# Kernel tuning notes

Measured on AMD Instinct MI355X. Metric: run time of the kernel, lower is better.

The kernel has to match this reference:

```python
import jax, jax.numpy as jnp
import numpy as np

USER_NUM = 100_000
ITEM_NUM = 50_000
N = USER_NUM + ITEM_NUM          # total nodes in the bipartite graph
HIDDEN = 64
LAYERS = 3
BATCH = 4096
NNZ = 4_800_000                  # ~avg degree 32


def setup_inputs() -> dict:
    key = jax.random.key(0)
    ks = jax.random.split(key, 7)
    emb = jax.random.normal(ks[0], (N, HIDDEN), dtype=jnp.float32) * 0.02
    rows = jax.random.randint(ks[1], (NNZ,), 0, N, dtype=jnp.int32)
    cols = jax.random.randint(ks[2], (NNZ,), 0, N, dtype=jnp.int32)
    # normalized-laplacian-like positive values, scaled ~ 1/avg_degree
    vals = jax.random.uniform(ks[3], (NNZ,), dtype=jnp.float32) * (1.0 / 32.0)
    user = jax.random.randint(ks[4], (BATCH,), 0, USER_NUM, dtype=jnp.int32)
    pos = jax.random.randint(ks[5], (BATCH,), USER_NUM, N, dtype=jnp.int32)
    neg = jax.random.randint(ks[6], (BATCH,), USER_NUM, N, dtype=jnp.int32)
    return {"emb": emb, "vals": vals, "rows": rows, "cols": cols,
            "user": user, "pos": pos, "neg": neg}


def _spmm(rows, cols, vals, x):
    # sparse [N,N] @ dense [N,d] in COO form: gather + scale + segment-sum
    return jax.ops.segment_sum(vals[:, None] * x[cols], rows, num_segments=N)


def reference(emb, vals, rows, cols, user, pos, neg):
    # layer-0 gathers
    user_acc = emb[user]
    pos_acc = emb[pos]
    neg_acc = emb[neg]
    e = emb
    for _ in range(LAYERS):
        e = _spmm(rows, cols, vals, e)
        user_acc = user_acc + e[user]
        pos_acc = pos_acc + e[pos]
        neg_acc = neg_acc + e[neg]
    denom = jnp.float32(LAYERS + 1)
    u = user_acc / denom   # mean over stacked layers
    p = pos_acc / denom
    n = neg_acc / denom
    pos_logits = jnp.einsum('id,id->i', u, p)
    neg_logits = jnp.einsum('id,id->i', u, n)
    # -log(sigmoid(x)) == -log_sigmoid(x) (numerically stable)
    loss = -jax.nn.log_sigmoid(pos_logits - neg_logits)
    return loss.sum()
```

## Files before the change

kernel.cpp:

```cpp
#include <hip/hip_runtime.h>

#define HIDDEN 64
#define PAD 96
#define CHUNK 8192
#define NBMAX 640
#define CAP 9600
#define S_SCALE 64.0f
#define INV_S 0.015625f

typedef unsigned int uint;
typedef unsigned char uchar;

__device__ __forceinline__ ushort f2bf(float f) {
    uint u = __float_as_uint(f);
    u = (u + 0x7FFFu + ((u >> 16) & 1u)) >> 16;
    return (ushort)u;
}
__device__ __forceinline__ float bf2f(ushort h) {
    return __uint_as_float(((uint)h) << 16);
}

#if __has_builtin(__builtin_amdgcn_cvt_pk_fp8_f32) && __has_builtin(__builtin_amdgcn_cvt_pk_f32_fp8)
#define FP8_HW 1
#else
#define FP8_HW 0
#endif

__device__ __forceinline__ uint enc8(float a, float b, float c, float d) {
#if FP8_HW
    int r = __builtin_amdgcn_cvt_pk_fp8_f32(a, b, 0, false);
    r = __builtin_amdgcn_cvt_pk_fp8_f32(c, d, r, true);
    return (uint)r;
#else
    auto enc1 = [](float x) -> uint {
        uint u = __float_as_uint(x);
        uint s = (u >> 24) & 0x80u;
        float af = fabsf(x);
        if (af < 0.015625f) return s;
        if (af >= 448.f) return s | 0x7Eu;
        uint bits = u & 0x7FFFFFFFu;
        bits -= (120u << 23);
        uint r = (bits + 0x7FFFFu + ((bits >> 20) & 1u)) >> 20;
        if (r > 0x7Eu) r = 0x7Eu;
        return s | r;
    };
    return enc1(a) | (enc1(b) << 8) | (enc1(c) << 16) | (enc1(d) << 24);
#endif
}

__device__ __forceinline__ float4 dec8(uint u) {
#if FP8_HW
    auto lo = __builtin_amdgcn_cvt_pk_f32_fp8((int)u, false);
    auto hi = __builtin_amdgcn_cvt_pk_f32_fp8((int)u, true);
    return make_float4(lo[0], lo[1], hi[0], hi[1]);
#else
    auto dec1 = [](uint b) -> float {
        uint m = b & 0x7Fu;
        uint s = (b & 0x80u) << 24;
        uint bits = m ? (s | ((m + 960u) << 20)) : s;
        return __uint_as_float(bits);
    };
    return make_float4(dec1(u & 0xFF), dec1((u >> 8) & 0xFF),
                       dec1((u >> 16) & 0xFF), dec1((u >> 24) & 0xFF));
#endif
}


__global__ void __launch_bounds__(256) k_f2fp8(const float4* __restrict__ src,
                                               uint2* __restrict__ dst, int n8) {
    int i = blockIdx.x * blockDim.x + threadIdx.x;
    if (i >= n8) return;
    float4 f0 = src[2 * i], f1 = src[2 * i + 1];
    uint2 o;
    o.x = enc8(f0.x * S_SCALE, f0.y * S_SCALE, f0.z * S_SCALE, f0.w * S_SCALE);
    o.y = enc8(f1.x * S_SCALE, f1.y * S_SCALE, f1.z * S_SCALE, f1.w * S_SCALE);
    dst[i] = o;
}


__global__ void __launch_bounds__(512) k_stage(const int* __restrict__ rows,
                                               const int* __restrict__ cols,
                                               const float* __restrict__ vals,
                                               int* __restrict__ cursor,
                                               int2* __restrict__ staged,
                                               int nnz, int nb) {
    __shared__ int  hS[NBMAX];
    __shared__ int  lsS[NBMAX];
    __shared__ int  gsS[NBMAX];
    __shared__ int  lcS[NBMAX];
    __shared__ int  ps[512];
    __shared__ int2 stg[CHUNK];

    int t  = threadIdx.x;
    int cb = blockIdx.x * CHUNK;

    for (int k = t; k < nb; k += 512) hS[k] = 0;
    __syncthreads();

    int4 ra[4];
    #pragma unroll
    for (int j = 0; j < 4; ++j) {
        int idx = cb + j * 2048 + t * 4;
        int4 r4;
        if (idx + 3 < nnz) {
            r4 = *(const int4*)(rows + idx);
        } else {
            r4.x = (idx     < nnz) ? rows[idx]     : -1;
            r4.y = (idx + 1 < nnz) ? rows[idx + 1] : -1;
            r4.z = (idx + 2 < nnz) ? rows[idx + 2] : -1;
            r4.w = (idx + 3 < nnz) ? rows[idx + 3] : -1;
        }
        ra[j] = r4;
        if (r4.x >= 0) atomicAdd(&hS[r4.x >> 8], 1);
        if (r4.y >= 0) atomicAdd(&hS[r4.y >> 8], 1);
        if (r4.z >= 0) atomicAdd(&hS[r4.z >> 8], 1);
        if (r4.w >= 0) atomicAdd(&hS[r4.w >> 8], 1);
    }
    __syncthreads();

    int k0 = 2 * t, k1 = 2 * t + 1;
    int c0 = (k0 < nb) ? hS[k0] : 0;
    int c1 = (k1 < nb) ? hS[k1] : 0;
    ps[t] = c0 + c1;
    __syncthreads();
    for (int d = 1; d < 512; d <<= 1) {
        int p = (t >= d) ? ps[t - d] : 0;
        __syncthreads();
        ps[t] += p;
        __syncthreads();
    }
    int excl = ps[t] - (c0 + c1);
    if (k0 < nb) { lsS[k0] = excl;      gsS[k0] = atomicAdd(&cursor[k0], c0); }
    if (k1 < nb) { lsS[k1] = excl + c0; gsS[k1] = atomicAdd(&cursor[k1], c1); }
    __syncthreads();
    for (int k = t; k < nb; k += 512) lcS[k] = lsS[k];
    __syncthreads();

    #pragma unroll
    for (int j = 0; j < 4; ++j) {
        int idx = cb + j * 2048 + t * 4;
        int4 r4 = ra[j];
        int4 c4; float4 v4;
        if (idx + 3 < nnz) {
            c4 = *(const int4*)(cols + idx);
            v4 = *(const float4*)(vals + idx);
        } else {
            c4.x = (idx     < nnz) ? cols[idx]     : 0;
            c4.y = (idx + 1 < nnz) ? cols[idx + 1] : 0;
            c4.z = (idx + 2 < nnz) ? cols[idx + 2] : 0;
            c4.w = (idx + 3 < nnz) ? cols[idx + 3] : 0;
            v4.x = (idx     < nnz) ? vals[idx]     : 0.f;
            v4.y = (idx + 1 < nnz) ? vals[idx + 1] : 0.f;
            v4.z = (idx + 2 < nnz) ? vals[idx + 2] : 0.f;
            v4.w = (idx + 3 < nnz) ? vals[idx + 3] : 0.f;
        }
        if (r4.x >= 0) { int s = atomicAdd(&lcS[r4.x >> 8], 1);
            stg[s] = make_int2(c4.x | ((r4.x & 255) << 18), __float_as_int(v4.x)); }
        if (r4.y >= 0) { int s = atomicAdd(&lcS[r4.y >> 8], 1);
            stg[s] = make_int2(c4.y | ((r4.y & 255) << 18), __float_as_int(v4.y)); }
        if (r4.z >= 0) { int s = atomicAdd(&lcS[r4.z >> 8], 1);
            stg[s] = make_int2(c4.z | ((r4.z & 255) << 18), __float_as_int(v4.z)); }
        if (r4.w >= 0) { int s = atomicAdd(&lcS[r4.w >> 8], 1);
            stg[s] = make_int2(c4.w | ((r4.w & 255) << 18), __float_as_int(v4.w)); }
    }
    __syncthreads();

    int m_total = nnz - cb; if (m_total > CHUNK) m_total = CHUNK;
    for (int i = t; i < m_total; i += 512) {
        int2 e = stg[i];
        int lo = 0, hi = nb - 1;
        while (lo < hi) {
            int mid = (lo + hi + 1) >> 1;
            if (lsS[mid] <= i) lo = mid; else hi = mid - 1;
        }
        int k = lo;
        int pos = gsS[k] + (i - lsS[k]);
        if (pos < CAP) staged[(size_t)k * CAP + pos] = e;
    }
}

__global__ void __launch_bounds__(1024) k_fine(const int2* __restrict__ staged,
                                               const int* __restrict__ stagecnt,
                                               int* __restrict__ cols_ell,
                                               ushort* __restrict__ vals_ell,
                                               int* __restrict__ cnt, int n) {
    __shared__ int2 out[CAP];
    __shared__ int hist[256], rstart[256], cursor[256], s2[256];
    int k = blockIdx.x;
    int t = threadIdx.x;
    size_t s0 = (size_t)k * CAP;
    int ck = stagecnt[k]; if (ck > CAP) ck = CAP;
    if (t < 256) hist[t] = 0;
    __syncthreads();
    for (int i = t; i < ck; i += 1024)
        atomicAdd(&hist[((uint)staged[s0 + i].x) >> 18], 1);
    __syncthreads();
    if (t < 256) s2[t] = hist[t];
    __syncthreads();
    for (int d = 1; d < 256; d <<= 1) {
        int p = (t < 256 && t >= d) ? s2[t - d] : 0;
        __syncthreads();
        if (t < 256) s2[t] += p;
        __syncthreads();
    }
    if (t < 256) {
        int rs = s2[t] - hist[t];
        rstart[t] = rs;
        cursor[t] = rs;
        int row = (k << 8) + t;
        if (row < n) cnt[row] = hist[t];
    }
    __syncthreads();
    for (int i = t; i < ck; i += 1024) {
        int2 e = staged[s0 + i];
        int lr = ((uint)e.x) >> 18;
        int slot = atomicAdd(&cursor[lr], 1);
        if (slot < CAP) out[slot] = make_int2(e.x & 0x3FFFF, e.y);
    }
    __syncthreads();
    for (int idx = t; idx < 256 * PAD; idx += 1024) {
        int lr = idx / PAD, j = idx - lr * PAD;
        if (j < hist[lr]) {
            int row = (k << 8) + lr;
            int2 o = out[rstart[lr] + j];
            cols_ell[(size_t)row * PAD + j] = o.x;
            vals_ell[(size_t)row * PAD + j] = f2bf(__int_as_float(o.y));
        }
    }
}


__device__ __forceinline__ float4 spmm_row4(const int* __restrict__ cnt,
                                            const int* __restrict__ cols_ell,
                                            const ushort* __restrict__ vals_ell,
                                            const uchar* __restrict__ x,
                                            int row, int lane) {
    int len = cnt[row]; if (len > PAD) len = PAD;
    const int*    cbp = cols_ell + (size_t)row * PAD;
    const ushort* vbp = vals_ell + (size_t)row * PAD;
    int g4 = (lane & 15) * 4;
    int e = lane >> 4;
    float a0 = 0.f, a1 = 0.f, a2 = 0.f, a3 = 0.f;
    float b0 = 0.f, b1 = 0.f, b2 = 0.f, b3 = 0.f;
    for (int j0 = 0; j0 < len; j0 += 64) {
        int m = len - j0; if (m > 64) m = 64;
        int c = 0; float v = 0.f;
        if (lane < m) {
            c = cbp[j0 + lane];
            v = bf2f(vbp[j0 + lane]);
        }
        int steps = (m + 3) >> 2;
        int s = 0;
        for (; s + 1 < steps; s += 2) {
            int   i0 = 4 * s + e,  i1 = 4 * s + 4 + e;
            int   c0 = __shfl(c, i0); float v0 = __shfl(v, i0);
            int   c1 = __shfl(c, i1); float v1 = __shfl(v, i1);
            uint u0 = *(const uint*)(x + ((size_t)c0 << 6) + g4);
            uint u1 = *(const uint*)(x + ((size_t)c1 << 6) + g4);
            float4 x0 = dec8(u0);
            float4 x1 = dec8(u1);
            a0 += v0 * x0.x; a1 += v0 * x0.y; a2 += v0 * x0.z; a3 += v0 * x0.w;
            b0 += v1 * x1.x; b1 += v1 * x1.y; b2 += v1 * x1.z; b3 += v1 * x1.w;
        }
        if (s < steps) {
            int i0 = 4 * s + e;
            int c0 = __shfl(c, i0); float v0 = __shfl(v, i0);
            uint u0 = *(const uint*)(x + ((size_t)c0 << 6) + g4);
            float4 x0 = dec8(u0);
            a0 += v0 * x0.x; a1 += v0 * x0.y; a2 += v0 * x0.z; a3 += v0 * x0.w;
        }
    }
    a0 += b0; a1 += b1; a2 += b2; a3 += b3;
    a0 += __shfl_xor(a0, 16); a1 += __shfl_xor(a1, 16);
    a2 += __shfl_xor(a2, 16); a3 += __shfl_xor(a3, 16);
    a0 += __shfl_xor(a0, 32); a1 += __shfl_xor(a1, 32);
    a2 += __shfl_xor(a2, 32); a3 += __shfl_xor(a3, 32);
    return make_float4(a0, a1, a2, a3);
}

__global__ void __launch_bounds__(256) k_spmm(const int* __restrict__ cnt,
                                              const int* __restrict__ cols_ell,
                                              const ushort* __restrict__ vals_ell,
                                              const uchar* __restrict__ x,
                                              uchar* __restrict__ y, int n) {
    int row  = (int)((blockIdx.x * blockDim.x + threadIdx.x) >> 6);
    int lane = threadIdx.x & 63;
    if (row >= n) return;
    float4 a = spmm_row4(cnt, cols_ell, vals_ell, x, row, lane);
    if (lane < 16) {
        uint r = enc8(a.x, a.y, a.z, a.w);
        *(uint*)(y + ((size_t)row << 6) + lane * 4) = r;
    }
}

__global__ void __launch_bounds__(256) k_spmm_batch(const int* __restrict__ cnt,
                                                    const int* __restrict__ cols_ell,
                                                    const ushort* __restrict__ vals_ell,
                                                    const uchar* __restrict__ x,
                                                    const int* __restrict__ user,
                                                    const int* __restrict__ pos,
                                                    const int* __restrict__ neg,
                                                    int batch, float* __restrict__ acc) {
    int slot = (int)((blockIdx.x * blockDim.x + threadIdx.x) >> 6);
    int lane = threadIdx.x & 63;
    if (slot >= 3 * batch) return;
    int which = slot / batch, i = slot - which * batch;
    const int* sel = (which == 0) ? user : (which == 1 ? pos : neg);
    float4 a = spmm_row4(cnt, cols_ell, vals_ell, x, sel[i], lane);
    if (lane < 16) {
        float4* p = (float4*)(acc + (size_t)slot * HIDDEN + lane * 4);
        float4 old = *p;
        old.x += a.x * INV_S; old.y += a.y * INV_S;
        old.z += a.z * INV_S; old.w += a.w * INV_S;
        *p = old;
    }
}


__global__ void __launch_bounds__(256) k_gather0(const float* __restrict__ e,
                                                 const int* __restrict__ user,
                                                 const int* __restrict__ pos,
                                                 const int* __restrict__ neg,
                                                 int batch, float* __restrict__ acc) {
    int row  = (int)((blockIdx.x * blockDim.x + threadIdx.x) >> 6);
    int lane = threadIdx.x & 63;
    if (row >= 3 * batch) return;
    int which = row / batch, i = row - which * batch;
    const int* sel = (which == 0) ? user : (which == 1 ? pos : neg);
    int s = sel[i];
    acc[(size_t)row * HIDDEN + lane] = e[(size_t)s * HIDDEN + lane];
}

__global__ void __launch_bounds__(256) k_gather8(const uchar* __restrict__ e,
                                                 const int* __restrict__ user,
                                                 const int* __restrict__ pos,
                                                 const int* __restrict__ neg,
                                                 int batch, float* __restrict__ acc) {
    int t    = blockIdx.x * blockDim.x + threadIdx.x;
    int wv   = t >> 6;
    int lane = threadIdx.x & 63;
    int row  = wv * 4 + (lane >> 4);
    if (row >= 3 * batch) return;
    int which = row / batch, i = row - which * batch;
    const int* sel = (which == 0) ? user : (which == 1 ? pos : neg);
    int s = sel[i];
    int g4 = (lane & 15) * 4;
    uint u = *(const uint*)(e + ((size_t)s << 6) + g4);
    float4 d = dec8(u);
    float4* p = (float4*)(acc + (size_t)row * HIDDEN + g4);
    float4 old = *p;
    old.x += d.x * INV_S; old.y += d.y * INV_S;
    old.z += d.z * INV_S; old.w += d.w * INV_S;
    *p = old;
}


__global__ void __launch_bounds__(256) k_loss(const float* __restrict__ acc, int batch,
                                              float* __restrict__ out) {
    int i    = (int)((blockIdx.x * blockDim.x + threadIdx.x) >> 6);
    int lane = threadIdx.x & 63;
    if (i >= batch) return;
    float u  = acc[(size_t)i * HIDDEN + lane] * 0.25f;
    float p  = acc[(size_t)(i + batch) * HIDDEN + lane] * 0.25f;
    float nn = acc[(size_t)(i + 2 * batch) * HIDDEN + lane] * 0.25f;
    float sp = u * p, sn = u * nn;
    for (int d = 32; d > 0; d >>= 1) {
        sp += __shfl_down(sp, d);
        sn += __shfl_down(sn, d);
    }
    if (lane == 0) {
        float z = sn - sp;
        float loss = fmaxf(z, 0.f) + log1pf(expf(-fabsf(z)));
        atomicAdd(out, loss);
    }
}


extern "C" void kernel_launch(void* const* d_in, const int* in_sizes, int n_in,
                              void* d_out, int out_size, void* d_ws, size_t ws_size,
                              hipStream_t stream) {
    (void)n_in; (void)out_size; (void)ws_size;
    const float* emb  = (const float*)d_in[0];
    const float* vals = (const float*)d_in[1];
    const int*   rows = (const int*)d_in[2];
    const int*   cols = (const int*)d_in[3];
    const int*   user = (const int*)d_in[4];
    const int*   pos  = (const int*)d_in[5];
    const int*   neg  = (const int*)d_in[6];

    const int n     = in_sizes[0] / HIDDEN;
    const int nnz   = in_sizes[1];
    const int batch = in_sizes[4];

    const int nb   = (n + 255) >> 8;
    const int nblk = (nnz + CHUNK - 1) / CHUNK;

    auto align256 = [](size_t x) { return (x + 255) & ~(size_t)255; };
    char* w = (char*)d_ws;
    int*    cnt      = (int*)w;    w += align256(sizeof(int)    * (size_t)n);
    int*    cursor   = (int*)w;    w += align256(sizeof(int)    * (size_t)NBMAX);
    int*    cols_ell = (int*)w;    w += align256(sizeof(int)    * (size_t)n * PAD);
    ushort* vals_ell = (ushort*)w; w += align256(sizeof(ushort) * (size_t)n * PAD);
    uchar*  emb8     = (uchar*)w;  w += align256((size_t)n * HIDDEN);
    uchar*  e0       = (uchar*)w;  w += align256((size_t)n * HIDDEN);
    uchar*  e1       = (uchar*)w;  w += align256((size_t)n * HIDDEN);
    float*  acc      = (float*)w;  w += align256(sizeof(float)  * (size_t)3 * batch * HIDDEN);
    int2*   staged   = (int2*)w;   w += align256(sizeof(int2)   * (size_t)nb * CAP);

    float* out = (float*)d_out;

    const int B = 256;
    dim3 blk(B);
    int g_conv = (n * HIDDEN / 8 + B - 1) / B;
    int g_spmm = (n + 3) / 4;
    int g_gath = (3 * batch + 3) / 4;
    int g_g8   = ((3 * batch + 3) / 4 * 64 + B - 1) / B;
    int g_loss = (batch + 3) / 4;

    hipMemsetAsync(cursor, 0, sizeof(int) * (size_t)NBMAX, stream);
    k_stage<<<nblk, 512, 0, stream>>>(rows, cols, vals, cursor, staged, nnz, nb);
    k_fine<<<nb, 1024, 0, stream>>>(staged, cursor, cols_ell, vals_ell, cnt, n);

    k_f2fp8<<<g_conv, blk, 0, stream>>>((const float4*)emb, (uint2*)emb8, n * HIDDEN / 8);

    hipMemsetAsync(out, 0, sizeof(float), stream);

    k_gather0<<<g_gath, blk, 0, stream>>>(emb, user, pos, neg, batch, acc);
    k_spmm<<<g_spmm, blk, 0, stream>>>(cnt, cols_ell, vals_ell, emb8, e0, n);
    k_gather8<<<g_g8, blk, 0, stream>>>(e0, user, pos, neg, batch, acc);
    k_spmm<<<g_spmm, blk, 0, stream>>>(cnt, cols_ell, vals_ell, e0, e1, n);
    k_gather8<<<g_g8, blk, 0, stream>>>(e1, user, pos, neg, batch, acc);
    k_spmm_batch<<<g_gath, blk, 0, stream>>>(cnt, cols_ell, vals_ell, e1, user, pos, neg, batch, acc);

    k_loss<<<g_loss, blk, 0, stream>>>(acc, batch, out);
}
```

Before: 325.0 us.

## Shrink staged COO entries to uint meta plus bf16 value, widen stage blocks

The staging kernel now converts values to bf16 early and writes them in a separate ushort array next to a uint metadata array, instead of int2 pairs. This cuts the bytes written and read through the intermediate staged buffer and the shared memory it uses. The stage kernel runs with 1024 threads and two int4 loads per thread instead of 512 threads and four. The SpMM inner loop is unrolled to four gathers per iteration to expose more memory-level parallelism, at the cost of more registers.

```diff
diff --git a/kernel.cpp b/kernel.cpp
--- a/kernel.cpp
+++ b/kernel.cpp
@@ -78,29 +78,31 @@
 }
 
 
-__global__ void __launch_bounds__(512) k_stage(const int* __restrict__ rows,
-                                               const int* __restrict__ cols,
-                                               const float* __restrict__ vals,
-                                               int* __restrict__ cursor,
-                                               int2* __restrict__ staged,
-                                               int nnz, int nb) {
-    __shared__ int  hS[NBMAX];
-    __shared__ int  lsS[NBMAX];
-    __shared__ int  gsS[NBMAX];
-    __shared__ int  lcS[NBMAX];
-    __shared__ int  ps[512];
-    __shared__ int2 stg[CHUNK];
+__global__ void __launch_bounds__(1024) k_stage(const int* __restrict__ rows,
+                                                const int* __restrict__ cols,
+                                                const float* __restrict__ vals,
+                                                int* __restrict__ cursor,
+                                                uint* __restrict__ smeta,
+                                                ushort* __restrict__ sval,
+                                                int nnz, int nb) {
+    __shared__ int    hS[NBMAX];
+    __shared__ int    lsS[NBMAX];
+    __shared__ int    gsS[NBMAX];
+    __shared__ int    lcS[NBMAX];
+    __shared__ int    ps[1024];
+    __shared__ uint   stgm[CHUNK];
+    __shared__ ushort stgv[CHUNK];
 
     int t  = threadIdx.x;
     int cb = blockIdx.x * CHUNK;
 
-    for (int k = t; k < nb; k += 512) hS[k] = 0;
-    __syncthreads();
-
-    int4 ra[4];
+    for (int k = t; k < nb; k += 1024) hS[k] = 0;
+    __syncthreads();
+
+    int4 ra[2];
     #pragma unroll
-    for (int j = 0; j < 4; ++j) {
-        int idx = cb + j * 2048 + t * 4;
+    for (int j = 0; j < 2; ++j) {
+        int idx = cb + j * 4096 + t * 4;
         int4 r4;
         if (idx + 3 < nnz) {
             r4 = *(const int4*)(rows + idx);
@@ -123,7 +125,7 @@
     int c1 = (k1 < nb) ? hS[k1] : 0;
     ps[t] = c0 + c1;
     __syncthreads();
-    for (int d = 1; d < 512; d <<= 1) {
+    for (int d = 1; d < 1024; d <<= 1) {
         int p = (t >= d) ? ps[t - d] : 0;
         __syncthreads();
         ps[t] += p;
@@ -133,12 +135,12 @@
     if (k0 < nb) { lsS[k0] = excl;      gsS[k0] = atomicAdd(&cursor[k0], c0); }
     if (k1 < nb) { lsS[k1] = excl + c0; gsS[k1] = atomicAdd(&cursor[k1], c1); }
     __syncthreads();
-    for (int k = t; k < nb; k += 512) lcS[k] = lsS[k];
+    for (int k = t; k < nb; k += 1024) lcS[k] = lsS[k];
     __syncthreads();
 
     #pragma unroll
-    for (int j = 0; j < 4; ++j) {
-        int idx = cb + j * 2048 + t * 4;
+    for (int j = 0; j < 2; ++j) {
+        int idx = cb + j * 4096 + t * 4;
         int4 r4 = ra[j];
         int4 c4; float4 v4;
         if (idx + 3 < nnz) {
@@ -155,19 +157,18 @@
             v4.w = (idx + 3 < nnz) ? vals[idx + 3] : 0.f;
         }
         if (r4.x >= 0) { int s = atomicAdd(&lcS[r4.x >> 8], 1);
-            stg[s] = make_int2(c4.x | ((r4.x & 255) << 18), __float_as_int(v4.x)); }
+            stgm[s] = (uint)c4.x | ((uint)(r4.x & 255) << 18); stgv[s] = f2bf(v4.x); }
         if (r4.y >= 0) { int s = atomicAdd(&lcS[r4.y >> 8], 1);
-            stg[s] = make_int2(c4.y | ((r4.y & 255) << 18), __float_as_int(v4.y)); }
+            stgm[s] = (uint)c4.y | ((uint)(r4.y & 255) << 18); stgv[s] = f2bf(v4.y); }
         if (r4.z >= 0) { int s = atomicAdd(&lcS[r4.z >> 8], 1);
-            stg[s] = make_int2(c4.z | ((r4.z & 255) << 18), __float_as_int(v4.z)); }
+            stgm[s] = (uint)c4.z | ((uint)(r4.z & 255) << 18); stgv[s] = f2bf(v4.z); }
         if (r4.w >= 0) { int s = atomicAdd(&lcS[r4.w >> 8], 1);
-            stg[s] = make_int2(c4.w | ((r4.w & 255) << 18), __float_as_int(v4.w)); }
+            stgm[s] = (uint)c4.w | ((uint)(r4.w & 255) << 18); stgv[s] = f2bf(v4.w); }
     }
     __syncthreads();
 
     int m_total = nnz - cb; if (m_total > CHUNK) m_total = CHUNK;
-    for (int i = t; i < m_total; i += 512) {
-        int2 e = stg[i];
+    for (int i = t; i < m_total; i += 1024) {
         int lo = 0, hi = nb - 1;
         while (lo < hi) {
             int mid = (lo + hi + 1) >> 1;
@@ -175,16 +176,21 @@
         }
         int k = lo;
         int pos = gsS[k] + (i - lsS[k]);
-        if (pos < CAP) staged[(size_t)k * CAP + pos] = e;
-    }
-}
-
-__global__ void __launch_bounds__(1024) k_fine(const int2* __restrict__ staged,
+        if (pos < CAP) {
+            smeta[(size_t)k * CAP + pos] = stgm[i];
+            sval [(size_t)k * CAP + pos] = stgv[i];
+        }
+    }
+}
+
+__global__ void __launch_bounds__(1024) k_fine(const uint* __restrict__ smeta,
+                                               const ushort* __restrict__ sval,
                                                const int* __restrict__ stagecnt,
                                                int* __restrict__ cols_ell,
                                                ushort* __restrict__ vals_ell,
                                                int* __restrict__ cnt, int n) {
-    __shared__ int2 out[CAP];
+    __shared__ uint   out_m[CAP];
+    __shared__ ushort out_v[CAP];
     __shared__ int hist[256], rstart[256], cursor[256], s2[256];
     int k = blockIdx.x;
     int t = threadIdx.x;
@@ -193,7 +199,7 @@
     if (t < 256) hist[t] = 0;
     __syncthreads();
     for (int i = t; i < ck; i += 1024)
-        atomicAdd(&hist[((uint)staged[s0 + i].x) >> 18], 1);
+        atomicAdd(&hist[smeta[s0 + i] >> 18], 1);
     __syncthreads();
     if (t < 256) s2[t] = hist[t];
     __syncthreads();
@@ -212,19 +218,19 @@
     }
     __syncthreads();
     for (int i = t; i < ck; i += 1024) {
-        int2 e = staged[s0 + i];
-        int lr = ((uint)e.x) >> 18;
+        uint m = smeta[s0 + i];
+        ushort v = sval[s0 + i];
+        int lr = (int)(m >> 18);
         int slot = atomicAdd(&cursor[lr], 1);
-        if (slot < CAP) out[slot] = make_int2(e.x & 0x3FFFF, e.y);
+        if (slot < CAP) { out_m[slot] = m & 0x3FFFFu; out_v[slot] = v; }
     }
     __syncthreads();
     for (int idx = t; idx < 256 * PAD; idx += 1024) {
         int lr = idx / PAD, j = idx - lr * PAD;
         if (j < hist[lr]) {
             int row = (k << 8) + lr;
-            int2 o = out[rstart[lr] + j];
-            cols_ell[(size_t)row * PAD + j] = o.x;
-            vals_ell[(size_t)row * PAD + j] = f2bf(__int_as_float(o.y));
+            cols_ell[(size_t)row * PAD + j] = (int)out_m[rstart[lr] + j];
+            vals_ell[(size_t)row * PAD + j] = out_v[rstart[lr] + j];
         }
     }
 }
@@ -251,18 +257,24 @@
         }
         int steps = (m + 3) >> 2;
         int s = 0;
-        for (; s + 1 < steps; s += 2) {
-            int   i0 = 4 * s + e,  i1 = 4 * s + 4 + e;
-            int   c0 = __shfl(c, i0); float v0 = __shfl(v, i0);
-            int   c1 = __shfl(c, i1); float v1 = __shfl(v, i1);
+        for (; s + 3 < steps; s += 4) {
+            int i0 = 4 * s + e, i1 = i0 + 4, i2 = i0 + 8, i3 = i0 + 12;
+            int   c0 = __shfl(c, i0); int   c1 = __shfl(c, i1);
+            int   c2 = __shfl(c, i2); int   c3 = __shfl(c, i3);
+            float v0 = __shfl(v, i0); float v1 = __shfl(v, i1);
+            float v2 = __shfl(v, i2); float v3 = __shfl(v, i3);
             uint u0 = *(const uint*)(x + ((size_t)c0 << 6) + g4);
             uint u1 = *(const uint*)(x + ((size_t)c1 << 6) + g4);
-            float4 x0 = dec8(u0);
-            float4 x1 = dec8(u1);
+            uint u2 = *(const uint*)(x + ((size_t)c2 << 6) + g4);
+            uint u3 = *(const uint*)(x + ((size_t)c3 << 6) + g4);
+            float4 x0 = dec8(u0); float4 x1 = dec8(u1);
+            float4 x2 = dec8(u2); float4 x3 = dec8(u3);
             a0 += v0 * x0.x; a1 += v0 * x0.y; a2 += v0 * x0.z; a3 += v0 * x0.w;
             b0 += v1 * x1.x; b1 += v1 * x1.y; b2 += v1 * x1.z; b3 += v1 * x1.w;
-        }
-        if (s < steps) {
+            a0 += v2 * x2.x; a1 += v2 * x2.y; a2 += v2 * x2.z; a3 += v2 * x2.w;
+            b0 += v3 * x3.x; b1 += v3 * x3.y; b2 += v3 * x3.z; b3 += v3 * x3.w;
+        }
+        for (; s < steps; ++s) {
             int i0 = 4 * s + e;
             int c0 = __shfl(c, i0); float v0 = __shfl(v, i0);
             uint u0 = *(const uint*)(x + ((size_t)c0 << 6) + g4);
@@ -405,7 +417,8 @@
     uchar*  e0       = (uchar*)w;  w += align256((size_t)n * HIDDEN);
     uchar*  e1       = (uchar*)w;  w += align256((size_t)n * HIDDEN);
     float*  acc      = (float*)w;  w += align256(sizeof(float)  * (size_t)3 * batch * HIDDEN);
-    int2*   staged   = (int2*)w;   w += align256(sizeof(int2)   * (size_t)nb * CAP);
+    uint*   smeta    = (uint*)w;   w += align256(sizeof(uint)   * (size_t)nb * CAP);
+    ushort* sval     = (ushort*)w; w += align256(sizeof(ushort) * (size_t)nb * CAP);
 
     float* out = (float*)d_out;
 
@@ -418,8 +431,8 @@
     int g_loss = (batch + 3) / 4;
 
     hipMemsetAsync(cursor, 0, sizeof(int) * (size_t)NBMAX, stream);
-    k_stage<<<nblk, 512, 0, stream>>>(rows, cols, vals, cursor, staged, nnz, nb);
-    k_fine<<<nb, 1024, 0, stream>>>(staged, cursor, cols_ell, vals_ell, cnt, n);
+    k_stage<<<nblk, 1024, 0, stream>>>(rows, cols, vals, cursor, smeta, sval, nnz, nb);
+    k_fine<<<nb, 1024, 0, stream>>>(smeta, sval, cursor, cols_ell, vals_ell, cnt, n);
 
     k_f2fp8<<<g_conv, blk, 0, stream>>>((const float4*)emb, (uint2*)emb8, n * HIDDEN / 8);
 
```

Measured after the change: 304.7 us. 1.07x faster.
